# Kernel optimization log

Measured on AMD Instinct MI355X. Metric: run time of the kernel, lower is better.

## Reference

```python
import jax, jax.numpy as jnp
import numpy as np

D_MODEL = 1024
N_HEADS = 16
HEAD_DIM = D_MODEL // N_HEADS


def setup_inputs() -> dict:
    key = jax.random.key(0)
    ks = jax.random.split(key, 9)
    s = 1.0 / np.sqrt(D_MODEL)
    x = jax.random.normal(ks[0], (2, 2048, D_MODEL), dtype=jnp.float32)
    Wq = jax.random.uniform(ks[1], (D_MODEL, D_MODEL), jnp.float32, -s, s)
    bq = jax.random.uniform(ks[2], (D_MODEL,), jnp.float32, -s, s)
    Wk = jax.random.uniform(ks[3], (D_MODEL, D_MODEL), jnp.float32, -s, s)
    bk = jax.random.uniform(ks[4], (D_MODEL,), jnp.float32, -s, s)
    Wv = jax.random.uniform(ks[5], (D_MODEL, D_MODEL), jnp.float32, -s, s)
    bv = jax.random.uniform(ks[6], (D_MODEL,), jnp.float32, -s, s)
    Wo = jax.random.uniform(ks[7], (D_MODEL, D_MODEL), jnp.float32, -s, s)
    bo = jax.random.uniform(ks[8], (D_MODEL,), jnp.float32, -s, s)
    return {"x": x, "Wq": Wq, "bq": bq, "Wk": Wk, "bk": bk,
            "Wv": Wv, "bv": bv, "Wo": Wo, "bo": bo}


def reference(x, Wq, bq, Wk, bk, Wv, bv, Wo, bo):
    B, L, _ = x.shape
    # Linear projections (torch Linear: y = x @ W.T + b; here W stored as [in, out])
    def split_heads(t):  # [B, L, D] -> [B, H, L, hd]
        return t.reshape(B, L, N_HEADS, HEAD_DIM).transpose(0, 2, 1, 3)
    Q = split_heads(x @ Wq + bq)
    K = split_heads(x @ Wk + bk)
    V = split_heads(x @ Wv + bv)
    scores = jnp.einsum('bhqd,bhkd->bhqk', Q, K) / np.sqrt(HEAD_DIM).astype(np.float32)
    attn = jax.nn.softmax(scores, axis=-1)
    out = jnp.einsum('bhqk,bhkd->bhqd', attn, V)
    out = out.transpose(0, 2, 1, 3).reshape(B, L, D_MODEL)
    return out @ Wo + bo
```

## Files before the change

### kernel.cpp

```cpp
#include <hip/hip_runtime.h>

typedef float f32x4  __attribute__((ext_vector_type(4)));
typedef short s16x8  __attribute__((ext_vector_type(8)));
typedef short s16x4  __attribute__((ext_vector_type(4)));
typedef unsigned short u16x8 __attribute__((ext_vector_type(8)));
typedef unsigned int   u32x2 __attribute__((ext_vector_type(2)));
typedef unsigned int   u32x4 __attribute__((ext_vector_type(4)));

#define DM   1024
#define LSEQ 2048
#define NH   16
#define HD   64
#define MTOT 4096
#define RS   3072

__device__ __forceinline__ unsigned short f2bf(float f) {
  union { float f; unsigned int u; } v; v.f = f;
  unsigned int r = (v.u + 0x7fffu + ((v.u >> 16) & 1u)) >> 16;
  return (unsigned short)r;
}

__device__ __forceinline__ unsigned cvtpk(float lo, float hi) {
  unsigned r;
  asm volatile("v_cvt_pk_bf16_f32 %0, %1, %2" : "=v"(r) : "v"(lo), "v"(hi));
  return r;
}
__device__ __forceinline__ s16x8 cvt8(float4 a, float4 b) {
  u32x4 o = {cvtpk(a.x, a.y), cvtpk(a.z, a.w), cvtpk(b.x, b.y), cvtpk(b.z, b.w)};
  return __builtin_bit_cast(s16x8, o);
}

__global__ __launch_bounds__(256) void wtrans4(const float* __restrict__ W0,
                                               const float* __restrict__ W1,
                                               const float* __restrict__ W2,
                                               const float* __restrict__ W3,
                                               unsigned short* __restrict__ Wt) {
  __shared__ __align__(16) unsigned short t[64][72];
  const int z = blockIdx.z;
  const float* W = (z == 0) ? W0 : (z == 1) ? W1 : (z == 2) ? W2 : W3;
  unsigned short* dst = Wt + (size_t)z * DM * DM;
  const int n0 = blockIdx.x * 64, k0 = blockIdx.y * 64;
  const int r = threadIdx.x >> 4, c4 = (threadIdx.x & 15) * 4;
#pragma unroll
  for (int rr = r; rr < 64; rr += 16) {
    float4 v = *(const float4*)&W[(long)(k0 + rr) * DM + n0 + c4];
    ushort4 u;
    u.x = f2bf(v.x); u.y = f2bf(v.y); u.z = f2bf(v.z); u.w = f2bf(v.w);
    *(ushort4*)&t[rr][c4] = u;
  }
  __syncthreads();
#pragma unroll
  for (int rr = r; rr < 64; rr += 16) {
    ushort4 u;
    u.x = t[c4 + 0][rr]; u.y = t[c4 + 1][rr];
    u.z = t[c4 + 2][rr]; u.w = t[c4 + 3][rr];
    *(ushort4*)&dst[(long)(n0 + rr) * DM + k0 + c4] = u;
  }
}

__global__ __launch_bounds__(256) void vtrans(const unsigned short* __restrict__ QKV,
                                              unsigned short* __restrict__ VT) {
  __shared__ __align__(16) unsigned short t[64][72];
  const int bh = blockIdx.y, st = blockIdx.x;
  const int b = bh >> 4, h = bh & 15;
  const int r = threadIdx.x >> 3, c8 = (threadIdx.x & 7) * 8;
#pragma unroll
  for (int rr = r; rr < 64; rr += 32) {
    const unsigned short* Vg = QKV + (size_t)(b * LSEQ + st * 64 + rr) * RS + 2 * DM + h * HD;
    *(u16x8*)&t[rr][c8] = *(const u16x8*)&Vg[c8];
  }
  __syncthreads();
  unsigned short* Vo = VT + (size_t)(bh * HD) * LSEQ + st * 64;
#pragma unroll
  for (int rr = r; rr < 64; rr += 32) {
    u16x8 u;
#pragma unroll
    for (int j = 0; j < 8; ++j) u[j] = t[c8 + j][rr];
    *(u16x8*)&Vo[(size_t)rr * LSEQ + c8] = u;
  }
}

template <int QKV_MODE>
__global__ __launch_bounds__(256) void gemm_bt(
    const void* __restrict__ Aptr, const unsigned short* __restrict__ Bt,
    const float* __restrict__ bias0, const float* __restrict__ bias1,
    const float* __restrict__ bias2, void* __restrict__ Cout, int N, int K) {
  __shared__ __align__(16) unsigned short As[128][72];
  __shared__ __align__(16) unsigned short Bs[128][72];
  const int tid = threadIdx.x;
  const int lane = tid & 63, w = tid >> 6;
  const int r16 = lane & 15, g = lane >> 4;
  const int m0 = blockIdx.y * 128, n0 = blockIdx.x * 128;
  const int wm = (w >> 1) * 64, wn = (w & 1) * 64;
  const int srow = tid >> 2, scol = (tid & 3) * 8;
  const float* Agf = (const float*)Aptr + (long)(m0 + srow) * K + scol;
  const unsigned short* Agh = (const unsigned short*)Aptr + (long)(m0 + srow) * K + scol;
  const unsigned short* Bg = Bt + (long)(n0 + srow) * K + scol;
  f32x4 acc[4][4] = {};
  float4 fa0, fa1, fa2, fa3, fa4, fa5, fa6, fa7;
  s16x8 a0, a1, a2, a3, b0, b1, b2, b3;

#define GLOAD_AB(koff)                                                        \
  {                                                                           \
    if constexpr (QKV_MODE) {                                                 \
      const float* p = Agf + (koff);                                          \
      fa0 = *(const float4*)p;        fa1 = *(const float4*)(p + 4);          \
      fa2 = *(const float4*)(p + 32); fa3 = *(const float4*)(p + 36);         \
      const float* q = p + 64L * K;                                           \
      fa4 = *(const float4*)q;        fa5 = *(const float4*)(q + 4);          \
      fa6 = *(const float4*)(q + 32); fa7 = *(const float4*)(q + 36);         \
    } else {                                                                  \
      const unsigned short* p = Agh + (koff);                                 \
      a0 = *(const s16x8*)p;             a1 = *(const s16x8*)(p + 32);        \
      a2 = *(const s16x8*)(p + 64L * K); a3 = *(const s16x8*)(p + 64L * K + 32); \
    }                                                                         \
    const unsigned short* pb = Bg + (koff);                                   \
    b0 = *(const s16x8*)pb;             b1 = *(const s16x8*)(pb + 32);        \
    b2 = *(const s16x8*)(pb + 64L * K); b3 = *(const s16x8*)(pb + 64L * K + 32); \
  }

  GLOAD_AB(0);
  for (int kt = 0; kt < K; kt += 64) {
    __syncthreads();
    if constexpr (QKV_MODE) {
      *(s16x8*)&As[srow][scol]           = cvt8(fa0, fa1);
      *(s16x8*)&As[srow][scol + 32]      = cvt8(fa2, fa3);
      *(s16x8*)&As[srow + 64][scol]      = cvt8(fa4, fa5);
      *(s16x8*)&As[srow + 64][scol + 32] = cvt8(fa6, fa7);
    } else {
      *(s16x8*)&As[srow][scol]           = a0;
      *(s16x8*)&As[srow][scol + 32]      = a1;
      *(s16x8*)&As[srow + 64][scol]      = a2;
      *(s16x8*)&As[srow + 64][scol + 32] = a3;
    }
    *(s16x8*)&Bs[srow][scol]           = b0;
    *(s16x8*)&Bs[srow][scol + 32]      = b1;
    *(s16x8*)&Bs[srow + 64][scol]      = b2;
    *(s16x8*)&Bs[srow + 64][scol + 32] = b3;
    __syncthreads();
    if (kt + 64 < K) GLOAD_AB(kt + 64);
#pragma unroll
    for (int kk = 0; kk < 64; kk += 32) {
      s16x8 af[4], bf[4];
#pragma unroll
      for (int i = 0; i < 4; i++) af[i] = *(const s16x8*)&As[wm + i * 16 + r16][kk + g * 8];
#pragma unroll
      for (int j = 0; j < 4; j++) bf[j] = *(const s16x8*)&Bs[wn + j * 16 + r16][kk + g * 8];
#pragma unroll
      for (int i = 0; i < 4; i++)
#pragma unroll
        for (int j = 0; j < 4; j++)
          acc[i][j] = __builtin_amdgcn_mfma_f32_16x16x32_bf16(af[i], bf[j], acc[i][j], 0, 0, 0);
    }
  }
#undef GLOAD_AB
#pragma unroll
  for (int i = 0; i < 4; i++) {
#pragma unroll
    for (int j = 0; j < 4; j++) {
      const int row = m0 + wm + i * 16 + g * 4;
      const int col = n0 + wn + j * 16 + r16;
      float bb, sc = 1.0f;
      if constexpr (QKV_MODE) {
        bb = (col < 1024) ? bias0[col] : (col < 2048) ? bias1[col - 1024] : bias2[col - 2048];
        if (col < 1024) sc = 0.18033688011112042f;
      } else {
        bb = bias0[col];
      }
#pragma unroll
      for (int r = 0; r < 4; r++) {
        float v = (acc[i][j][r] + bb) * sc;
        if constexpr (QKV_MODE)
          ((unsigned short*)Cout)[(long)(row + r) * N + col] = f2bf(v);
        else
          ((float*)Cout)[(long)(row + r) * N + col] = v;
      }
    }
  }
}

__global__ __launch_bounds__(512) void attn9(const unsigned short* __restrict__ QKV,
                                             const unsigned short* __restrict__ VT,
                                             unsigned short* __restrict__ O) {
  __shared__ __align__(16) unsigned short Ks[2][2][64][76];
  __shared__ __align__(16) unsigned short Vs[2][2][64][76];
  __shared__ float Lsum[4][32];
  const int tid = threadIdx.x;
  const int lane = tid & 63, w = tid >> 6;
  const int wq = w & 3;
  const int hb = tid >> 8;
  const int r16 = lane & 15, g = lane >> 4;
  const int qb = blockIdx.x, bh = blockIdx.y;
  const int b = bh >> 4, h = bh & 15;

  const unsigned short* QgA =
      QKV + (size_t)(b * LSEQ + qb * 128 + wq * 32 + r16) * RS + h * HD;
  const unsigned short* QgB = QgA + 16 * RS;
  const s16x8 qa0 = *(const s16x8*)&QgA[g * 8];
  const s16x8 qa1 = *(const s16x8*)&QgA[32 + g * 8];
  const s16x8 qb0 = *(const s16x8*)&QgB[g * 8];
  const s16x8 qb1 = *(const s16x8*)&QgB[32 + g * 8];

  const unsigned short* Kb =
      QKV + (size_t)(b * LSEQ + hb * 1024) * RS + DM + h * HD;
  const unsigned short* Vb =
      VT + (size_t)(bh * HD) * LSEQ + hb * 1024;
  const int t256 = tid & 255;
  const int srow = t256 >> 2, scol = (t256 & 3) * 8;

  f32x4 oA[4] = {}, oB[4] = {};
  float psA[4] = {0.f, 0.f, 0.f, 0.f};
  float psB[4] = {0.f, 0.f, 0.f, 0.f};

  s16x8 k0 = *(const s16x8*)&Kb[(size_t)srow * RS + scol];
  s16x8 k1 = *(const s16x8*)&Kb[(size_t)srow * RS + scol + 32];
  s16x8 v0 = *(const s16x8*)&Vb[(size_t)srow * LSEQ + scol];
  s16x8 v1 = *(const s16x8*)&Vb[(size_t)srow * LSEQ + scol + 32];
  *(s16x8*)&Ks[hb][0][srow][scol]      = k0;
  *(s16x8*)&Ks[hb][0][srow][scol + 32] = k1;
  *(s16x8*)&Vs[hb][0][srow][scol]      = v0;
  *(s16x8*)&Vs[hb][0][srow][scol + 32] = v1;
  __syncthreads();

  for (int tt = 0; tt < 16; ++tt) {
    const int cur = tt & 1;
    if (tt + 1 < 16) {
      const size_t ko = (size_t)((tt + 1) * 64 + srow) * RS + scol;
      const size_t vo = (size_t)srow * LSEQ + (tt + 1) * 64 + scol;
      k0 = *(const s16x8*)&Kb[ko];
      k1 = *(const s16x8*)&Kb[ko + 32];
      v0 = *(const s16x8*)&Vb[vo];
      v1 = *(const s16x8*)&Vb[vo + 32];
    }

    f32x4 sA[4], sB[4];
#pragma unroll
    for (int kc = 0; kc < 4; kc++) {
      s16x8 kb0 = *(const s16x8*)&Ks[hb][cur][kc * 16 + r16][g * 8];
      s16x8 kb1 = *(const s16x8*)&Ks[hb][cur][kc * 16 + r16][32 + g * 8];
      f32x4 zA = {}, zB = {};
      zA = __builtin_amdgcn_mfma_f32_16x16x32_bf16(kb0, qa0, zA, 0, 0, 0);
      sA[kc] = __builtin_amdgcn_mfma_f32_16x16x32_bf16(kb1, qa1, zA, 0, 0, 0);
      zB = __builtin_amdgcn_mfma_f32_16x16x32_bf16(kb0, qb0, zB, 0, 0, 0);
      sB[kc] = __builtin_amdgcn_mfma_f32_16x16x32_bf16(kb1, qb1, zB, 0, 0, 0);
    }

    s16x4 paA[4], paB[4];
#pragma unroll
    for (int kc = 0; kc < 4; kc++) {
      float a0f = exp2f(sA[kc][0]);
      float a1f = exp2f(sA[kc][1]);
      float a2f = exp2f(sA[kc][2]);
      float a3f = exp2f(sA[kc][3]);
      psA[0] += a0f; psA[1] += a1f; psA[2] += a2f; psA[3] += a3f;
      u32x2 pkA = {cvtpk(a0f, a1f), cvtpk(a2f, a3f)};
      paA[kc] = __builtin_bit_cast(s16x4, pkA);
      float b0f = exp2f(sB[kc][0]);
      float b1f = exp2f(sB[kc][1]);
      float b2f = exp2f(sB[kc][2]);
      float b3f = exp2f(sB[kc][3]);
      psB[0] += b0f; psB[1] += b1f; psB[2] += b2f; psB[3] += b3f;
      u32x2 pkB = {cvtpk(b0f, b1f), cvtpk(b2f, b3f)};
      paB[kc] = __builtin_bit_cast(s16x4, pkB);
    }

#pragma unroll
    for (int kc = 0; kc < 4; kc++)
#pragma unroll
      for (int dc = 0; dc < 4; dc++) {
        s16x4 vb = *(const s16x4*)&Vs[hb][cur][dc * 16 + r16][kc * 16 + 4 * g];
        oA[dc] = __builtin_amdgcn_mfma_f32_16x16x16bf16_1k(paA[kc], vb, oA[dc], 0, 0, 0);
        oB[dc] = __builtin_amdgcn_mfma_f32_16x16x16bf16_1k(paB[kc], vb, oB[dc], 0, 0, 0);
      }

    if (tt + 1 < 16) {
      *(s16x8*)&Ks[hb][cur ^ 1][srow][scol]      = k0;
      *(s16x8*)&Ks[hb][cur ^ 1][srow][scol + 32] = k1;
      *(s16x8*)&Vs[hb][cur ^ 1][srow][scol]      = v0;
      *(s16x8*)&Vs[hb][cur ^ 1][srow][scol + 32] = v1;
      __syncthreads();
    }
  }

  __syncthreads();
  float (*xo)[33] = reinterpret_cast<float(*)[33]>(&Ks[0][0][0][0]);
  float (*xs)[9]  = reinterpret_cast<float(*)[9]>(&Vs[0][0][0][0]);
  if (w >= 4) {
    const int l = tid & 255;
#pragma unroll
    for (int dc = 0; dc < 4; dc++) {
      *(f32x4*)&xo[l][4 * dc]      = oA[dc];
      *(f32x4*)&xo[l][16 + 4 * dc] = oB[dc];
    }
#pragma unroll
    for (int r = 0; r < 4; r++) { xs[l][r] = psA[r]; xs[l][4 + r] = psB[r]; }
  }
  __syncthreads();
  float totA = 0.f, totB = 0.f;
  if (w < 4) {
    const int l = tid;
#pragma unroll
    for (int dc = 0; dc < 4; dc++) {
      oA[dc] += *(const f32x4*)&xo[l][4 * dc];
      oB[dc] += *(const f32x4*)&xo[l][16 + 4 * dc];
    }
#pragma unroll
    for (int r = 0; r < 4; r++) { psA[r] += xs[l][r]; psB[r] += xs[l][4 + r]; }
    totA = psA[0] + psA[1] + psA[2] + psA[3];
    totA += __shfl_xor(totA, 16);
    totA += __shfl_xor(totA, 32);
    totB = psB[0] + psB[1] + psB[2] + psB[3];
    totB += __shfl_xor(totB, 16);
    totB += __shfl_xor(totB, 32);
    if (g == 0) {
      Lsum[wq][r16]      = totA;
      Lsum[wq][16 + r16] = totB;
    }
  }
  __syncthreads();
  if (w < 4) {
    const float4 svA = *(const float4*)&Lsum[wq][4 * g];
    const float4 svB = *(const float4*)&Lsum[wq][16 + 4 * g];
    unsigned short* Og = O + (size_t)(b * LSEQ + qb * 128 + wq * 32) * DM + h * HD;
#pragma unroll
    for (int r = 0; r < 4; r++) {
      const float invA = 1.0f / ((const float*)&svA)[r];
      const float invB = 1.0f / ((const float*)&svB)[r];
#pragma unroll
      for (int dc = 0; dc < 4; dc++) {
        Og[(size_t)(g * 4 + r) * DM + dc * 16 + r16]      = f2bf(oA[dc][r] * invA);
        Og[(size_t)(16 + g * 4 + r) * DM + dc * 16 + r16] = f2bf(oB[dc][r] * invB);
      }
    }
  }
}

extern "C" void kernel_launch(void* const* d_in, const int* in_sizes, int n_in,
                              void* d_out, int out_size, void* d_ws, size_t ws_size,
                              hipStream_t stream) {
  const float* x  = (const float*)d_in[0];
  const float* Wq = (const float*)d_in[1];
  const float* bq = (const float*)d_in[2];
  const float* Wk = (const float*)d_in[3];
  const float* bk = (const float*)d_in[4];
  const float* Wv = (const float*)d_in[5];
  const float* bv = (const float*)d_in[6];
  const float* Wo = (const float*)d_in[7];
  const float* bo = (const float*)d_in[8];

  unsigned short* VTb  = (unsigned short*)d_ws;
  unsigned short* Wcat = VTb + (size_t)MTOT * DM;
  unsigned short* Wot  = Wcat + (size_t)3 * DM * DM;
  unsigned short* QKVb = Wot + (size_t)DM * DM;
  unsigned short* Ob   = QKVb + (size_t)MTOT * 3 * DM;

  wtrans4<<<dim3(16, 16, 4), 256, 0, stream>>>(Wq, Wk, Wv, Wo, Wcat);

  gemm_bt<1><<<dim3(3 * DM / 128, MTOT / 128), 256, 0, stream>>>(
      (const void*)x, Wcat, bq, bk, bv, (void*)QKVb, 3 * DM, DM);
  vtrans<<<dim3(LSEQ / 64, 2 * NH), 256, 0, stream>>>(QKVb, VTb);
  attn9<<<dim3(LSEQ / 128, 2 * NH), 512, 0, stream>>>(QKVb, VTb, Ob);
  gemm_bt<0><<<dim3(DM / 128, MTOT / 128), 256, 0, stream>>>(
      (const void*)Ob, Wot, bo, nullptr, nullptr, d_out, DM, DM);
}
```

Measured before the change: 146.8 us.

## Fuse V transpose into QKV GEMM epilogue and swap attention grid order

The QKV projection GEMM now writes the V columns straight into the transposed VT layout from its epilogue, so the separate vtrans kernel launch and its extra round trip through global memory are gone. The attention grid is also reordered so that batch-head varies fastest across blocks. That changes which blocks run together and may affect cache reuse of K/V. The epilogue writes for V become 8-byte strided stores along the sequence dimension, which coalesce less well than the row-major stores.

```diff
diff --git a/kernel.cpp b/kernel.cpp
--- a/kernel.cpp
+++ b/kernel.cpp
@@ -58,33 +58,12 @@
   }
 }
 
-__global__ __launch_bounds__(256) void vtrans(const unsigned short* __restrict__ QKV,
-                                              unsigned short* __restrict__ VT) {
-  __shared__ __align__(16) unsigned short t[64][72];
-  const int bh = blockIdx.y, st = blockIdx.x;
-  const int b = bh >> 4, h = bh & 15;
-  const int r = threadIdx.x >> 3, c8 = (threadIdx.x & 7) * 8;
-#pragma unroll
-  for (int rr = r; rr < 64; rr += 32) {
-    const unsigned short* Vg = QKV + (size_t)(b * LSEQ + st * 64 + rr) * RS + 2 * DM + h * HD;
-    *(u16x8*)&t[rr][c8] = *(const u16x8*)&Vg[c8];
-  }
-  __syncthreads();
-  unsigned short* Vo = VT + (size_t)(bh * HD) * LSEQ + st * 64;
-#pragma unroll
-  for (int rr = r; rr < 64; rr += 32) {
-    u16x8 u;
-#pragma unroll
-    for (int j = 0; j < 8; ++j) u[j] = t[c8 + j][rr];
-    *(u16x8*)&Vo[(size_t)rr * LSEQ + c8] = u;
-  }
-}
-
 template <int QKV_MODE>
 __global__ __launch_bounds__(256) void gemm_bt(
     const void* __restrict__ Aptr, const unsigned short* __restrict__ Bt,
     const float* __restrict__ bias0, const float* __restrict__ bias1,
-    const float* __restrict__ bias2, void* __restrict__ Cout, int N, int K) {
+    const float* __restrict__ bias2, void* __restrict__ Cout,
+    unsigned short* __restrict__ VT, int N, int K) {
   __shared__ __align__(16) unsigned short As[128][72];
   __shared__ __align__(16) unsigned short Bs[128][72];
   const int tid = threadIdx.x;
@@ -154,6 +133,27 @@
     }
   }
 #undef GLOAD_AB
+
+  if (QKV_MODE && n0 >= 2048) {
+#pragma unroll
+    for (int i = 0; i < 4; i++) {
+      const int row0 = m0 + wm + i * 16 + g * 4;
+      const int b = row0 >> 11, seq = row0 & 2047;
+#pragma unroll
+      for (int j = 0; j < 4; j++) {
+        const int cv = n0 + wn + j * 16 + r16 - 2048;
+        const float bb = bias2[cv];
+        const int bh = b * NH + (cv >> 6), d = cv & 63;
+        ushort4 u;
+        u.x = f2bf(acc[i][j][0] + bb);
+        u.y = f2bf(acc[i][j][1] + bb);
+        u.z = f2bf(acc[i][j][2] + bb);
+        u.w = f2bf(acc[i][j][3] + bb);
+        *(ushort4*)(VT + ((size_t)bh * HD + d) * LSEQ + seq) = u;
+      }
+    }
+    return;
+  }
 #pragma unroll
   for (int i = 0; i < 4; i++) {
 #pragma unroll
@@ -162,7 +162,7 @@
       const int col = n0 + wn + j * 16 + r16;
       float bb, sc = 1.0f;
       if constexpr (QKV_MODE) {
-        bb = (col < 1024) ? bias0[col] : (col < 2048) ? bias1[col - 1024] : bias2[col - 2048];
+        bb = (col < 1024) ? bias0[col] : bias1[col - 1024];
         if (col < 1024) sc = 0.18033688011112042f;
       } else {
         bb = bias0[col];
@@ -190,7 +190,7 @@
   const int wq = w & 3;
   const int hb = tid >> 8;
   const int r16 = lane & 15, g = lane >> 4;
-  const int qb = blockIdx.x, bh = blockIdx.y;
+  const int bh = blockIdx.x, qb = blockIdx.y;
   const int b = bh >> 4, h = bh & 15;
 
   const unsigned short* QgA =
@@ -357,9 +357,8 @@
   wtrans4<<<dim3(16, 16, 4), 256, 0, stream>>>(Wq, Wk, Wv, Wo, Wcat);
 
   gemm_bt<1><<<dim3(3 * DM / 128, MTOT / 128), 256, 0, stream>>>(
-      (const void*)x, Wcat, bq, bk, bv, (void*)QKVb, 3 * DM, DM);
-  vtrans<<<dim3(LSEQ / 64, 2 * NH), 256, 0, stream>>>(QKVb, VTb);
-  attn9<<<dim3(LSEQ / 128, 2 * NH), 512, 0, stream>>>(QKVb, VTb, Ob);
+      (const void*)x, Wcat, bq, bk, bv, (void*)QKVb, VTb, 3 * DM, DM);
+  attn9<<<dim3(2 * NH, LSEQ / 128), 512, 0, stream>>>(QKVb, VTb, Ob);
   gemm_bt<0><<<dim3(DM / 128, MTOT / 128), 256, 0, stream>>>(
-      (const void*)Ob, Wot, bo, nullptr, nullptr, d_out, DM, DM);
-}
+      (const void*)Ob, Wot, bo, nullptr, nullptr, d_out, nullptr, DM, DM);
+}
```

Result: faster. 136.8 us, median of 3 (-6.8%).
